# Kernel tuning notes

Measured on AMD Instinct MI355X. Metric: run time of the kernel, lower is better.

The kernel has to match this reference:

```python
import jax, jax.numpy as jnp
import numpy as np

jax.config.update("jax_enable_x64", True)

TOL = 1e-06


def setup_inputs() -> dict:
    key = jax.random.key(0)
    k1, k2 = jax.random.split(key)
    n, d = 4096, 128
    output = jax.random.normal(k1, (n, d), dtype=jnp.float32)
    # target: square roots of patristic distances -> nonnegative
    target = jax.random.uniform(k2, (n, n), dtype=jnp.float32) * 2.0
    return {"output": output, "target": target}


def reference(output, target):
    # Torch module casts to double before all math
    out = output.astype(jnp.float64)
    tgt = target.astype(jnp.float64)
    n = out.shape[0]

    # Lorentz inner product: B = outer(s, s) - out @ out.T, s = sqrt(1 + ||o||^2)
    s = jnp.sqrt(1.0 + jnp.sum(out * out, axis=1))          # [n]
    B = s[:, None] * s[None, :] - out @ out.T               # [n, n]

    # Clamp near-1 entries exactly to 1 (torch: B[(B-1).abs() < tol] = 1.0)
    clamp = jnp.abs(B - 1.0) < TOL
    # Safe acosh: evaluate at 2.0 where clamped to avoid inf/nan, then set dist=0 there
    B_safe = jnp.where(clamp, 2.0, B)
    dist = jnp.where(clamp, 0.0, jnp.arccosh(B_safe))       # acosh(1) == 0

    # Strictly-lower-triangular masked MAE
    tril_mask = jnp.tril(jnp.ones((n, n), dtype=jnp.float64), k=-1)
    loss = jnp.sum(jnp.abs(dist - tgt) * tril_mask) / (n * (n - 1))
    return loss
```

## Files before the change

kernel.cpp:

```cpp
#include <hip/hip_runtime.h>
#include <math.h>

#define N 4096
#define D 128
#define TS 64
#define NT (N / TS)
#define NBLK (NT * (NT + 1) / 2)
#define NG (N / 16)
#define TPAD 68

typedef __attribute__((ext_vector_type(8))) short short8;
typedef __attribute__((ext_vector_type(4))) float f32x4;

union frag_u { short8 v; unsigned int u[4]; };

__device__ __forceinline__ unsigned int pack_bf16x2(float a, float b) {
    unsigned int ua = __float_as_uint(a), ub = __float_as_uint(b);
    ua = (ua + 0x7FFFu + ((ua >> 16) & 1u)) >> 16;
    ub = (ub + 0x7FFFu + ((ub >> 16) & 1u)) >> 16;
    return ua | (ub << 16);
}

__global__ __launch_bounds__(256)
void prep_kernel(const float* __restrict__ O,
                 short8* __restrict__ Ofrag,
                 float* __restrict__ s) {
    __shared__ float psum[16][17];
    const int g    = blockIdx.x;
    const int tid  = threadIdx.x;
    const int kk   = tid >> 6;
    const int lane = tid & 63;
    const int r16  = lane & 15;
    const int qd   = lane >> 4;
    const float* src = O + (size_t)(g * 16 + r16) * D + kk * 32 + qd * 8;
    const float4 v0 = *(const float4*)(src);
    const float4 v1 = *(const float4*)(src + 4);
    frag_u f;
    f.u[0] = pack_bf16x2(v0.x, v0.y);
    f.u[1] = pack_bf16x2(v0.z, v0.w);
    f.u[2] = pack_bf16x2(v1.x, v1.y);
    f.u[3] = pack_bf16x2(v1.z, v1.w);
    Ofrag[(g * 4 + kk) * 64 + lane] = f.v;
    psum[kk * 4 + qd][r16] = v0.x * v0.x + v0.y * v0.y + v0.z * v0.z + v0.w * v0.w
                           + v1.x * v1.x + v1.y * v1.y + v1.z * v1.z + v1.w * v1.w;
    __syncthreads();
    if (tid < 16) {
        float acc = 1.0f;
        #pragma unroll
        for (int x = 0; x < 16; x++) acc += psum[x][tid];
        s[g * 16 + tid] = sqrtf(acc);
    }
}

__device__ __forceinline__ float acosh_dist(float B) {
    if (fabsf(B - 1.0f) < 1e-6f) return 0.0f;
    const float Bc = fmaxf(B, 1.0f);
    return __log2f(Bc + sqrtf(fmaf(Bc, Bc, -1.0f))) * 0.6931471805599453f;
}

__global__ __launch_bounds__(256, 4)
void tile_loss_kernel(const short8* __restrict__ Fr,
                      const float* __restrict__ s,
                      const float* __restrict__ tgt,
                      float* __restrict__ partials) {
    __shared__ float T[TS][TPAD];
    __shared__ float wsum[4];

    const int t = blockIdx.x;
    int ti = (int)((sqrtf(8.0f * (float)t + 1.0f) - 1.0f) * 0.5f);
    while ((ti + 1) * (ti + 2) / 2 <= t) ti++;
    while (ti * (ti + 1) / 2 > t) ti--;
    const int tj = t - ti * (ti + 1) / 2;

    const int tid  = threadIdx.x;
    const int wave = tid >> 6;
    const int lane = tid & 63;
    const int quad = lane >> 4;
    const int l16  = lane & 15;

    const int ib0 = ti * TS;
    const int jb  = tj * TS;

    {
        const int r = tid >> 4;
        const int c = (tid & 15) * 4;
        float4 tg[4];
        #pragma unroll
        for (int p = 0; p < 4; p++)
            tg[p] = *(const float4*)(tgt + (size_t)(ib0 + p * 16 + r) * N + jb + c);
        #pragma unroll
        for (int p = 0; p < 4; p++)
            *(float4*)&T[p * 16 + r][c] = tg[p];
    }

    float sj[4];
    #pragma unroll
    for (int n = 0; n < 4; n++) sj[n] = s[jb + n * 16 + l16];
    const int r0 = wave * 16 + quad * 4;
    float si[4];
    #pragma unroll
    for (int r = 0; r < 4; r++) si[r] = s[ib0 + r0 + r];

    f32x4 acc[4] = {};
    const int ga4 = (ti * 4 + wave) * 4;
    const int gb4 = tj * 4 * 4;
    #pragma unroll
    for (int kp = 0; kp < 2; kp++) {
        const int k0 = kp * 2, k1 = kp * 2 + 1;
        const short8 a0 = Fr[(ga4 + k0) * 64 + lane];
        const short8 a1 = Fr[(ga4 + k1) * 64 + lane];
        short8 b0[4], b1[4];
        #pragma unroll
        for (int n = 0; n < 4; n++) {
            b0[n] = Fr[(gb4 + n * 4 + k0) * 64 + lane];
            b1[n] = Fr[(gb4 + n * 4 + k1) * 64 + lane];
        }
        #pragma unroll
        for (int n = 0; n < 4; n++)
            acc[n] = __builtin_amdgcn_mfma_f32_16x16x32_bf16(a0, b0[n], acc[n], 0, 0, 0);
        #pragma unroll
        for (int n = 0; n < 4; n++)
            acc[n] = __builtin_amdgcn_mfma_f32_16x16x32_bf16(a1, b1[n], acc[n], 0, 0, 0);
    }

    __syncthreads();

    float lsum = 0.0f;
    if (ti != tj) {
        #pragma unroll
        for (int r = 0; r < 4; r++)
            #pragma unroll
            for (int n = 0; n < 4; n++) {
                const float B  = fmaf(si[r], sj[n], -acc[n][r]);
                const float tv = T[r0 + r][n * 16 + l16];
                lsum += fabsf(acosh_dist(B) - tv);
            }
    } else {
        #pragma unroll
        for (int r = 0; r < 4; r++) {
            const int i = ib0 + r0 + r;
            #pragma unroll
            for (int n = 0; n < 4; n++) {
                const int j = jb + n * 16 + l16;
                if (j < i) {
                    const float B  = fmaf(si[r], sj[n], -acc[n][r]);
                    const float tv = T[r0 + r][n * 16 + l16];
                    lsum += fabsf(acosh_dist(B) - tv);
                }
            }
        }
    }

    #pragma unroll
    for (int off = 32; off > 0; off >>= 1)
        lsum += __shfl_down(lsum, off, 64);
    if (lane == 0) wsum[wave] = lsum;
    __syncthreads();
    if (tid == 0)
        partials[t] = wsum[0] + wsum[1] + wsum[2] + wsum[3];
}

__global__ __launch_bounds__(256)
void final_reduce_kernel(const float* __restrict__ partials,
                         float* __restrict__ loss) {
    __shared__ float wsum[4];
    const int tid  = threadIdx.x;
    const int wave = tid >> 6;
    const int lane = tid & 63;
    float acc = 0.0f;
    for (int i = tid; i < NBLK; i += 256) acc += partials[i];
    #pragma unroll
    for (int off = 32; off > 0; off >>= 1)
        acc += __shfl_down(acc, off, 64);
    if (lane == 0) wsum[wave] = acc;
    __syncthreads();
    if (tid == 0) {
        const float tot = wsum[0] + wsum[1] + wsum[2] + wsum[3];
        loss[0] = tot * (1.0f / ((float)N * (float)(N - 1)));
    }
}

extern "C" void kernel_launch(void* const* d_in, const int* in_sizes, int n_in,
                              void* d_out, int out_size, void* d_ws, size_t ws_size,
                              hipStream_t stream) {
    const float* O   = (const float*)d_in[0];
    const float* tgt = (const float*)d_in[1];
    float* loss = (float*)d_out;

    short8* Ofrag = (short8*)d_ws;
    float* s        = (float*)((char*)d_ws + (size_t)N * D * 2);
    float* partials = s + N;

    prep_kernel<<<NG, 256, 0, stream>>>(O, Ofrag, s);
    tile_loss_kernel<<<NBLK, 256, 0, stream>>>(Ofrag, s, tgt, partials);
    final_reduce_kernel<<<1, 256, 0, stream>>>(partials, loss);
}
```

Baseline: 103.1 us.

## Use 128x128 block tiles with 64x64 per-wave subtiles and direct target loads

New measurement: 105.1 us. Within noise of the previous version (+2.0%).

```diff
diff --git a/kernel.cpp b/kernel.cpp
--- a/kernel.cpp
+++ b/kernel.cpp
@@ -3,11 +3,10 @@
 
 #define N 4096
 #define D 128
-#define TS 64
-#define NT (N / TS)
-#define NBLK (NT * (NT + 1) / 2)
+#define BT 128
+#define NT2 (N / BT)
+#define NBLK (NT2 * (NT2 + 1) / 2)
 #define NG (N / 16)
-#define TPAD 68
 
 typedef __attribute__((ext_vector_type(8))) short short8;
 typedef __attribute__((ext_vector_type(4))) float f32x4;
@@ -58,12 +57,11 @@
     return __log2f(Bc + sqrtf(fmaf(Bc, Bc, -1.0f))) * 0.6931471805599453f;
 }
 
-__global__ __launch_bounds__(256, 4)
+__global__ __launch_bounds__(256, 2)
 void tile_loss_kernel(const short8* __restrict__ Fr,
                       const float* __restrict__ s,
                       const float* __restrict__ tgt,
                       float* __restrict__ partials) {
-    __shared__ float T[TS][TPAD];
     __shared__ float wsum[4];
 
     const int t = blockIdx.x;
@@ -77,75 +75,72 @@
     const int lane = tid & 63;
     const int quad = lane >> 4;
     const int l16  = lane & 15;
+    const int mq   = wave >> 1;
+    const int nq   = wave & 1;
 
-    const int ib0 = ti * TS;
-    const int jb  = tj * TS;
-
-    {
-        const int r = tid >> 4;
-        const int c = (tid & 15) * 4;
-        float4 tg[4];
-        #pragma unroll
-        for (int p = 0; p < 4; p++)
-            tg[p] = *(const float4*)(tgt + (size_t)(ib0 + p * 16 + r) * N + jb + c);
-        #pragma unroll
-        for (int p = 0; p < 4; p++)
-            *(float4*)&T[p * 16 + r][c] = tg[p];
-    }
-
-    float sj[4];
-    #pragma unroll
-    for (int n = 0; n < 4; n++) sj[n] = s[jb + n * 16 + l16];
-    const int r0 = wave * 16 + quad * 4;
-    float si[4];
-    #pragma unroll
-    for (int r = 0; r < 4; r++) si[r] = s[ib0 + r0 + r];
-
-    f32x4 acc[4] = {};
-    const int ga4 = (ti * 4 + wave) * 4;
-    const int gb4 = tj * 4 * 4;
-    #pragma unroll
-    for (int kp = 0; kp < 2; kp++) {
-        const int k0 = kp * 2, k1 = kp * 2 + 1;
-        const short8 a0 = Fr[(ga4 + k0) * 64 + lane];
-        const short8 a1 = Fr[(ga4 + k1) * 64 + lane];
-        short8 b0[4], b1[4];
-        #pragma unroll
-        for (int n = 0; n < 4; n++) {
-            b0[n] = Fr[(gb4 + n * 4 + k0) * 64 + lane];
-            b1[n] = Fr[(gb4 + n * 4 + k1) * 64 + lane];
-        }
-        #pragma unroll
-        for (int n = 0; n < 4; n++)
-            acc[n] = __builtin_amdgcn_mfma_f32_16x16x32_bf16(a0, b0[n], acc[n], 0, 0, 0);
-        #pragma unroll
-        for (int n = 0; n < 4; n++)
-            acc[n] = __builtin_amdgcn_mfma_f32_16x16x32_bf16(a1, b1[n], acc[n], 0, 0, 0);
-    }
-
-    __syncthreads();
+    const bool diag   = (ti == tj);
+    const bool active = !(diag && mq == 0 && nq == 1);
+    const bool qdiag  = diag && (mq == nq);
 
     float lsum = 0.0f;
-    if (ti != tj) {
+    if (active) {
+        const int ib  = ti * BT + mq * 64;
+        const int jb  = tj * BT + nq * 64;
+        const int iag = ib >> 4;
+        const int jag = jb >> 4;
+
+        f32x4 acc[4][4] = {};
         #pragma unroll
-        for (int r = 0; r < 4; r++)
+        for (int kk = 0; kk < 4; kk++) {
+            short8 a[4], b[4];
             #pragma unroll
-            for (int n = 0; n < 4; n++) {
-                const float B  = fmaf(si[r], sj[n], -acc[n][r]);
-                const float tv = T[r0 + r][n * 16 + l16];
-                lsum += fabsf(acosh_dist(B) - tv);
+            for (int m = 0; m < 4; m++) a[m] = Fr[((iag + m) * 4 + kk) * 64 + lane];
+            #pragma unroll
+            for (int n = 0; n < 4; n++) b[n] = Fr[((jag + n) * 4 + kk) * 64 + lane];
+            #pragma unroll
+            for (int m = 0; m < 4; m++)
+                #pragma unroll
+                for (int n = 0; n < 4; n++)
+                    acc[m][n] = __builtin_amdgcn_mfma_f32_16x16x32_bf16(
+                        a[m], b[n], acc[m][n], 0, 0, 0);
+        }
+
+        float sj[4];
+        #pragma unroll
+        for (int n = 0; n < 4; n++) sj[n] = s[jb + n * 16 + l16];
+
+        #pragma unroll
+        for (int m = 0; m < 4; m++) {
+            const int i0 = ib + m * 16 + quad * 4;
+            float si[4], tv[4][4];
+            #pragma unroll
+            for (int r = 0; r < 4; r++) {
+                si[r] = s[i0 + r];
+                const float* trow = tgt + (size_t)(i0 + r) * N + jb;
+                #pragma unroll
+                for (int n = 0; n < 4; n++)
+                    tv[r][n] = trow[n * 16 + l16];
             }
-    } else {
-        #pragma unroll
-        for (int r = 0; r < 4; r++) {
-            const int i = ib0 + r0 + r;
-            #pragma unroll
-            for (int n = 0; n < 4; n++) {
-                const int j = jb + n * 16 + l16;
-                if (j < i) {
-                    const float B  = fmaf(si[r], sj[n], -acc[n][r]);
-                    const float tv = T[r0 + r][n * 16 + l16];
-                    lsum += fabsf(acosh_dist(B) - tv);
+            if (!qdiag) {
+                #pragma unroll
+                for (int r = 0; r < 4; r++)
+                    #pragma unroll
+                    for (int n = 0; n < 4; n++) {
+                        const float B = fmaf(si[r], sj[n], -acc[m][n][r]);
+                        lsum += fabsf(acosh_dist(B) - tv[r][n]);
+                    }
+            } else {
+                #pragma unroll
+                for (int r = 0; r < 4; r++) {
+                    const int i = i0 + r;
+                    #pragma unroll
+                    for (int n = 0; n < 4; n++) {
+                        const int j = jb + n * 16 + l16;
+                        if (j < i) {
+                            const float B = fmaf(si[r], sj[n], -acc[m][n][r]);
+                            lsum += fabsf(acosh_dist(B) - tv[r][n]);
+                        }
+                    }
                 }
             }
         }
```
